# Performance work log

Hardware: AMD Instinct MI355X
Metric: run time of the kernel (lower is better)

## Reference

```python
import jax, jax.numpy as jnp
import numpy as np

B, H, S, D = 4, 16, 2048, 64


def setup_inputs() -> dict:
    key = jax.random.key(0)
    kq, kk, kv = jax.random.split(key, 3)
    q = jax.random.normal(kq, (B, H, S, D), dtype=jnp.float32)
    k = jax.random.normal(kk, (B, H, S, D), dtype=jnp.float32)
    v = jax.random.normal(kv, (B, H, S, D), dtype=jnp.float32)
    # causal mask: 1 = keep, 0 = masked (matches masked_fill(mask == 0, -10000))
    mask = jnp.tril(jnp.ones((S, S), dtype=jnp.int32))[None, None, :, :]
    return {"q": q, "k": k, "v": v, "mask": mask}


def reference(q, k, v, mask):
    head_dim = q.shape[3]
    # [b,h,s,t] attention logits
    attn = jnp.einsum("bhsd,bhtd->bhst", q, k) / jnp.sqrt(jnp.float32(head_dim))
    attn = jnp.where(mask == 0, jnp.float32(-10000.0), attn)
    score = jax.nn.softmax(attn, axis=-1)
    # dropout is identity at inference (eval mode)
    return jnp.einsum("bhst,bhtd->bhsd", score, v)
```

## Files before the change

### kernel.cpp

```cpp
#include <hip/hip_runtime.h>
#include <hip/hip_bf16.h>

typedef __bf16 bf16_t;
typedef bf16_t bf16x8 __attribute__((ext_vector_type(8)));
typedef float  f32x4  __attribute__((ext_vector_type(4)));
typedef float  f32x16 __attribute__((ext_vector_type(16)));
typedef int    i32x4  __attribute__((ext_vector_type(4)));

#define DH 64

__device__ __forceinline__ unsigned pkbf(float a, float b) {
    union { bf16_t h[2]; unsigned u; } z;
    z.h[0] = (bf16_t)a; z.h[1] = (bf16_t)b;
    return z.u;
}

#if defined(__has_builtin)
#  if __has_builtin(__builtin_amdgcn_exp2f)
#    define EXP2F(x) __builtin_amdgcn_exp2f(x)
#  else
#    define EXP2F(x) __expf((x) * 0.69314718056f)
#  endif
#else
#  define EXP2F(x) __expf((x) * 0.69314718056f)
#endif


__global__ __launch_bounds__(256, 2)
void sdpa_fwd(const float* __restrict__ Qg, const float* __restrict__ Kg,
              const float* __restrict__ Vg, float* __restrict__ Og)
{
    __shared__ char lds[2 * 32768];

    const int n  = blockIdx.x;
    const int o  = ((n & 7) << 6) | (n >> 3);
    const int bh = o >> 3;
    const int pr = o & 7;

    const int t   = threadIdx.x;
    const int w   = t >> 6;
    const int l31 = t & 31;
    const int hi  = (t >> 5) & 1;
    const int swk0 = ((l31 ^ (l31 >> 3)) & 7) << 4;
    const int swk1 = (((32 + l31) ^ ((32 + l31) >> 3)) & 7) << 4;

    const size_t hoff = (size_t)bh * 2048 * DH;
    const float* Qh = Qg + hoff;
    const float* Kh = Kg + hoff;
    const float* Vh = Vg + hoff;
    float*       Oh = Og + hoff;

    const int srow = (t >> 3) * 2;
    const int sdc  = t & 7;

    const int p0  = 15 - pr;
    const int nk0 = 2 * p0 + 2;
    const int NS  = 17;

    f32x4 rk[8], rv[8];

    auto keybase = [&](int g) { return ((g < nk0) ? g : g - nk0) * 64; };

    auto loadT = [&](int key0, int half) {
        const float* kp = Kh + (size_t)(key0 + srow) * DH + sdc * 8;
        rk[half*4+0] = *(const f32x4*)kp;        rk[half*4+1] = *(const f32x4*)(kp + 4);
        rk[half*4+2] = *(const f32x4*)(kp + DH); rk[half*4+3] = *(const f32x4*)(kp + DH + 4);
        const float* vp = Vh + (size_t)(key0 + srow) * DH + sdc * 8;
        rv[half*4+0] = *(const f32x4*)vp;        rv[half*4+1] = *(const f32x4*)(vp + 4);
        rv[half*4+2] = *(const f32x4*)(vp + DH); rv[half*4+3] = *(const f32x4*)(vp + DH + 4);
    };
    auto stageT = [&](char* kb_, char* vb_, int half) {
#pragma unroll
        for (int r2 = 0; r2 < 2; ++r2) {
            const int key = srow + r2;
            union { unsigned u[4]; bf16x8 v; } f;
            f.u[0] = pkbf(rk[half*4+r2*2][0],   rk[half*4+r2*2][1]);
            f.u[1] = pkbf(rk[half*4+r2*2][2],   rk[half*4+r2*2][3]);
            f.u[2] = pkbf(rk[half*4+r2*2+1][0], rk[half*4+r2*2+1][1]);
            f.u[3] = pkbf(rk[half*4+r2*2+1][2], rk[half*4+r2*2+1][3]);
            *(bf16x8*)(kb_ + ((key * 128 + sdc * 16) ^ (((key ^ (key >> 3)) & 7) << 4))) = f.v;
        }
#pragma unroll
        for (int jj = 0; jj < 8; ++jj) {
            const int d  = sdc * 8 + jj;
            const float x0 = (jj < 4) ? rv[half*4+0][jj & 3] : rv[half*4+1][jj & 3];
            const float x1 = (jj < 4) ? rv[half*4+2][jj & 3] : rv[half*4+3][jj & 3];
            *(unsigned*)(vb_ + ((d * 128 + srow * 2) ^ (((jj ^ sdc) & 7) << 4)))
                = pkbf(x0, x1);
        }
    };

    const float QSCALE = 0.125f * 1.44269504088896f;

    loadT(keybase(0), 0); loadT(keybase(1), 1);
    stageT(lds, lds + 8192, 0);
    stageT(lds + 16384, lds + 24576, 1);
    loadT(keybase(2), 0); loadT(keybase(3), 1);
    __syncthreads();

    int gt = 0;
    const int stripes[2] = { p0, pr };
    for (int s = 0; s < 2; ++s) {
        const int p    = stripes[s];
        const int h    = 2 * p + 2;
        const int qsb  = p * 128 + w * 32;
        const int qrow = qsb + l31;
        const int ktd  = qsb >> 6;

        bf16x8 qf[4];
#pragma unroll
        for (int sd = 0; sd < 4; ++sd) {
            const float* qp = Qh + (size_t)qrow * DH + sd * 16 + hi * 8;
            f32x4 a = *(const f32x4*)qp;
            f32x4 b = *(const f32x4*)(qp + 4);
            union { unsigned u[4]; bf16x8 v; } f;
            f.u[0] = pkbf(a[0]*QSCALE, a[1]*QSCALE);
            f.u[1] = pkbf(a[2]*QSCALE, a[3]*QSCALE);
            f.u[2] = pkbf(b[0]*QSCALE, b[1]*QSCALE);
            f.u[3] = pkbf(b[2]*QSCALE, b[3]*QSCALE);
            qf[sd] = f.v;
        }

        f32x16 acc0 = {}, acc1 = {};
        float l_run = 0.0f;

        auto doTile = [&](char* kb_, char* vb_, int i) {
            f32x16 tf0 = {}, tf1 = {};
            __builtin_amdgcn_s_setprio(1);
#pragma unroll
            for (int sd = 0; sd < 4; ++sd) {
                const int inner = sd * 32 + hi * 16;
                const bf16x8 k0 = *(const bf16x8*)(kb_ + ((l31 * 128 + inner) ^ swk0));
                const bf16x8 k1 = *(const bf16x8*)(kb_ + (((32 + l31) * 128 + inner) ^ swk1));
                tf0 = __builtin_amdgcn_mfma_f32_32x32x16_bf16(k0, qf[sd], tf0, 0, 0, 0);
                tf1 = __builtin_amdgcn_mfma_f32_32x32x16_bf16(k1, qf[sd], tf1, 0, 0, 0);
            }
            __builtin_amdgcn_s_setprio(0);

            if (i == ktd) {
#pragma unroll
                for (int rr = 0; rr < 16; ++rr) {
                    const int krow = i * 64 + (rr & 3) + 8 * (rr >> 2) + 4 * hi;
                    if (krow > qrow)      tf0[rr] = -20000.0f;
                    if (krow + 32 > qrow) tf1[rr] = -20000.0f;
                }
            }

            float sum = 0.0f;
#pragma unroll
            for (int rr = 0; rr < 16; ++rr) { tf0[rr] = EXP2F(tf0[rr]); sum += tf0[rr]; }
#pragma unroll
            for (int rr = 0; rr < 16; ++rr) { tf1[rr] = EXP2F(tf1[rr]); sum += tf1[rr]; }
            sum += __shfl_xor(sum, 32);
            l_run += sum;

            unsigned P0[2][4], P1[2][4];
#pragma unroll
            for (int rg = 0; rg < 4; ++rg) {
                P0[0][rg] = pkbf(tf0[rg * 4 + 0], tf0[rg * 4 + 1]);
                P1[0][rg] = pkbf(tf0[rg * 4 + 2], tf0[rg * 4 + 3]);
                P0[1][rg] = pkbf(tf1[rg * 4 + 0], tf1[rg * 4 + 1]);
                P1[1][rg] = pkbf(tf1[rg * 4 + 2], tf1[rg * 4 + 3]);
            }

            __builtin_amdgcn_s_setprio(1);
#pragma unroll
            for (int sidx = 0; sidx < 4; ++sidx) {
                const int kb  = sidx >> 1;
                const int rgl = (sidx & 1) * 2, rgh = rgl + 1;
                int w0, w1, w2, w3;
#if defined(__has_builtin) && __has_builtin(__builtin_amdgcn_permlane32_swap)
                auto r0 = __builtin_amdgcn_permlane32_swap((int)P0[kb][rgl], (int)P0[kb][rgh], false, false);
                auto r1 = __builtin_amdgcn_permlane32_swap((int)P1[kb][rgl], (int)P1[kb][rgh], false, false);
                w0 = r0[0]; w2 = r0[1]; w1 = r1[0]; w3 = r1[1];
#else
                const int sa0 = __shfl_xor((int)P0[kb][rgl], 32);
                const int sb0 = __shfl_xor((int)P0[kb][rgh], 32);
                const int sa1 = __shfl_xor((int)P1[kb][rgl], 32);
                const int sb1 = __shfl_xor((int)P1[kb][rgh], 32);
                w0 = hi ? sb0 : (int)P0[kb][rgl];
                w2 = hi ? (int)P0[kb][rgh] : sa0;
                w1 = hi ? sb1 : (int)P1[kb][rgl];
                w3 = hi ? (int)P1[kb][rgh] : sa1;
#endif
                union { i32x4 ii; bf16x8 v; } pz;
                pz.ii = (i32x4){ w0, w1, w2, w3 };

                const int inner = sidx * 32 + hi * 16;
                const int d0 = l31;
                const int d1 = 32 + l31;
                const int sz0 = (((d0 & 7) ^ (d0 >> 3)) & 7) << 4;
                const int sz1 = (((d1 & 7) ^ (d1 >> 3)) & 7) << 4;
                const bf16x8 v0 = *(const bf16x8*)(vb_ + ((d0 * 128 + inner) ^ sz0));
                const bf16x8 v1 = *(const bf16x8*)(vb_ + ((d1 * 128 + inner) ^ sz1));
                acc0 = __builtin_amdgcn_mfma_f32_32x32x16_bf16(v0, pz.v, acc0, 0, 0, 0);
                acc1 = __builtin_amdgcn_mfma_f32_32x32x16_bf16(v1, pz.v, acc1, 0, 0, 0);
            }
            __builtin_amdgcn_s_setprio(0);
        };

        for (int si = 0; si < (h >> 1); ++si, gt += 2) {
            const int gs = gt >> 1;
            char* cb_ = lds + (gs & 1) * 32768;
            char* sb_ = lds + ((gs + 1) & 1) * 32768;

            if (gs + 1 < NS) {
                stageT(sb_, sb_ + 8192, 0);
                stageT(sb_ + 16384, sb_ + 24576, 1);
            }
            if (gs + 2 < NS) {
                loadT(keybase(2 * gs + 4), 0);
                loadT(keybase(2 * gs + 5), 1);
            }

            const int i0 = 2 * si;
            if (i0 <= ktd)     doTile(cb_,          cb_ + 8192,  i0);
            if (i0 + 1 <= ktd) doTile(cb_ + 16384,  cb_ + 24576, i0 + 1);

            __syncthreads();
        }

        const float inv = 1.0f / l_run;
        float* op = Oh + (size_t)qrow * DH;
#pragma unroll
        for (int rq = 0; rq < 4; ++rq) {
            f32x4 o0, o1;
#pragma unroll
            for (int j = 0; j < 4; ++j) {
                o0[j] = acc0[rq * 4 + j] * inv;
                o1[j] = acc1[rq * 4 + j] * inv;
            }
            *(f32x4*)(op + 8 * rq + 4 * hi)      = o0;
            *(f32x4*)(op + 32 + 8 * rq + 4 * hi) = o1;
        }
    }
}

extern "C" void kernel_launch(void* const* d_in, const int* in_sizes, int n_in,
                              void* d_out, int out_size, void* d_ws, size_t ws_size,
                              hipStream_t stream) {
    (void)in_sizes; (void)n_in; (void)d_ws; (void)ws_size; (void)out_size;
    const float* q = (const float*)d_in[0];
    const float* k = (const float*)d_in[1];
    const float* v = (const float*)d_in[2];
    float* out = (float*)d_out;
    hipLaunchKernelGGL(sdpa_fwd, dim3(512), dim3(256), 0, stream, q, k, v, out);
}
```

Before: 70.93 us.

## Process both causal query stripes in one shared K/V pass

Each block previously handled its long and short query stripes one after the other, loading and staging K/V tiles for each stripe separately, which meant 17 staged steps. Now both stripes' Q fragments and accumulators stay live and a single sweep over the K/V tiles feeds both stripes, so the short stripe's tiles are reused from LDS instead of being fetched and converted again. This removes redundant global loads, bf16 conversion and LDS staging. In exchange it doubles the accumulator and Q register footprint, which can cut occupancy or cause spills.

```diff
diff --git a/kernel.cpp b/kernel.cpp
--- a/kernel.cpp
+++ b/kernel.cpp
@@ -53,13 +53,12 @@
     const int srow = (t >> 3) * 2;
     const int sdc  = t & 7;
 
-    const int p0  = 15 - pr;
-    const int nk0 = 2 * p0 + 2;
-    const int NS  = 17;
+    const int pA  = 15 - pr;
+    const int pB  = pr;
+    const int NTt = 2 * pA + 2;
+    const int NS  = NTt >> 1;
 
     f32x4 rk[8], rv[8];
-
-    auto keybase = [&](int g) { return ((g < nk0) ? g : g - nk0) * 64; };
 
     auto loadT = [&](int key0, int half) {
         const float* kp = Kh + (size_t)(key0 + srow) * DH + sdc * 8;
@@ -92,143 +91,163 @@
 
     const float QSCALE = 0.125f * 1.44269504088896f;
 
-    loadT(keybase(0), 0); loadT(keybase(1), 1);
+    const int qsbA = pA * 128 + w * 32, qrowA = qsbA + l31, ktdA = qsbA >> 6;
+    const int qsbB = pB * 128 + w * 32, qrowB = qsbB + l31, ktdB = qsbB >> 6;
+
+    bf16x8 qfA[4], qfB[4];
+#pragma unroll
+    for (int sd = 0; sd < 4; ++sd) {
+        const float* qpA = Qh + (size_t)qrowA * DH + sd * 16 + hi * 8;
+        f32x4 a = *(const f32x4*)qpA;
+        f32x4 b = *(const f32x4*)(qpA + 4);
+        union { unsigned u[4]; bf16x8 v; } f;
+        f.u[0] = pkbf(a[0]*QSCALE, a[1]*QSCALE);
+        f.u[1] = pkbf(a[2]*QSCALE, a[3]*QSCALE);
+        f.u[2] = pkbf(b[0]*QSCALE, b[1]*QSCALE);
+        f.u[3] = pkbf(b[2]*QSCALE, b[3]*QSCALE);
+        qfA[sd] = f.v;
+        const float* qpB = Qh + (size_t)qrowB * DH + sd * 16 + hi * 8;
+        a = *(const f32x4*)qpB;
+        b = *(const f32x4*)(qpB + 4);
+        f.u[0] = pkbf(a[0]*QSCALE, a[1]*QSCALE);
+        f.u[1] = pkbf(a[2]*QSCALE, a[3]*QSCALE);
+        f.u[2] = pkbf(b[0]*QSCALE, b[1]*QSCALE);
+        f.u[3] = pkbf(b[2]*QSCALE, b[3]*QSCALE);
+        qfB[sd] = f.v;
+    }
+
+    f32x16 accA0 = {}, accA1 = {}, accB0 = {}, accB1 = {};
+    float lA = 0.0f, lB = 0.0f;
+
+    auto doTileS = [&](const bf16x8* qf, f32x16& acc0, f32x16& acc1, float& l_run,
+                       int ktd, int qrow, char* kb_, char* vb_, int i) {
+        f32x16 tf0 = {}, tf1 = {};
+        __builtin_amdgcn_s_setprio(1);
+#pragma unroll
+        for (int sd = 0; sd < 4; ++sd) {
+            const int inner = sd * 32 + hi * 16;
+            const bf16x8 k0 = *(const bf16x8*)(kb_ + ((l31 * 128 + inner) ^ swk0));
+            const bf16x8 k1 = *(const bf16x8*)(kb_ + (((32 + l31) * 128 + inner) ^ swk1));
+            tf0 = __builtin_amdgcn_mfma_f32_32x32x16_bf16(k0, qf[sd], tf0, 0, 0, 0);
+            tf1 = __builtin_amdgcn_mfma_f32_32x32x16_bf16(k1, qf[sd], tf1, 0, 0, 0);
+        }
+        __builtin_amdgcn_s_setprio(0);
+
+        if (i == ktd) {
+#pragma unroll
+            for (int rr = 0; rr < 16; ++rr) {
+                const int krow = i * 64 + (rr & 3) + 8 * (rr >> 2) + 4 * hi;
+                if (krow > qrow)      tf0[rr] = -20000.0f;
+                if (krow + 32 > qrow) tf1[rr] = -20000.0f;
+            }
+        }
+
+        float sum = 0.0f;
+#pragma unroll
+        for (int rr = 0; rr < 16; ++rr) { tf0[rr] = EXP2F(tf0[rr]); sum += tf0[rr]; }
+#pragma unroll
+        for (int rr = 0; rr < 16; ++rr) { tf1[rr] = EXP2F(tf1[rr]); sum += tf1[rr]; }
+        sum += __shfl_xor(sum, 32);
+        l_run += sum;
+
+        unsigned P0[2][4], P1[2][4];
+#pragma unroll
+        for (int rg = 0; rg < 4; ++rg) {
+            P0[0][rg] = pkbf(tf0[rg * 4 + 0], tf0[rg * 4 + 1]);
+            P1[0][rg] = pkbf(tf0[rg * 4 + 2], tf0[rg * 4 + 3]);
+            P0[1][rg] = pkbf(tf1[rg * 4 + 0], tf1[rg * 4 + 1]);
+            P1[1][rg] = pkbf(tf1[rg * 4 + 2], tf1[rg * 4 + 3]);
+        }
+
+        __builtin_amdgcn_s_setprio(1);
+#pragma unroll
+        for (int sidx = 0; sidx < 4; ++sidx) {
+            const int kb  = sidx >> 1;
+            const int rgl = (sidx & 1) * 2, rgh = rgl + 1;
+            int w0, w1, w2, w3;
+#if defined(__has_builtin) && __has_builtin(__builtin_amdgcn_permlane32_swap)
+            auto r0 = __builtin_amdgcn_permlane32_swap((int)P0[kb][rgl], (int)P0[kb][rgh], false, false);
+            auto r1 = __builtin_amdgcn_permlane32_swap((int)P1[kb][rgl], (int)P1[kb][rgh], false, false);
+            w0 = r0[0]; w2 = r0[1]; w1 = r1[0]; w3 = r1[1];
+#else
+            const int sa0 = __shfl_xor((int)P0[kb][rgl], 32);
+            const int sb0 = __shfl_xor((int)P0[kb][rgh], 32);
+            const int sa1 = __shfl_xor((int)P1[kb][rgl], 32);
+            const int sb1 = __shfl_xor((int)P1[kb][rgh], 32);
+            w0 = hi ? sb0 : (int)P0[kb][rgl];
+            w2 = hi ? (int)P0[kb][rgh] : sa0;
+            w1 = hi ? sb1 : (int)P1[kb][rgl];
+            w3 = hi ? (int)P1[kb][rgh] : sa1;
+#endif
+            union { i32x4 ii; bf16x8 v; } pz;
+            pz.ii = (i32x4){ w0, w1, w2, w3 };
+
+            const int inner = sidx * 32 + hi * 16;
+            const int d0 = l31;
+            const int d1 = 32 + l31;
+            const int sz0 = (((d0 & 7) ^ (d0 >> 3)) & 7) << 4;
+            const int sz1 = (((d1 & 7) ^ (d1 >> 3)) & 7) << 4;
+            const bf16x8 v0 = *(const bf16x8*)(vb_ + ((d0 * 128 + inner) ^ sz0));
+            const bf16x8 v1 = *(const bf16x8*)(vb_ + ((d1 * 128 + inner) ^ sz1));
+            acc0 = __builtin_amdgcn_mfma_f32_32x32x16_bf16(v0, pz.v, acc0, 0, 0, 0);
+            acc1 = __builtin_amdgcn_mfma_f32_32x32x16_bf16(v1, pz.v, acc1, 0, 0, 0);
+        }
+        __builtin_amdgcn_s_setprio(0);
+    };
+
+    loadT(0, 0);  loadT(64, 1);
     stageT(lds, lds + 8192, 0);
     stageT(lds + 16384, lds + 24576, 1);
-    loadT(keybase(2), 0); loadT(keybase(3), 1);
+    loadT(128, 0); loadT(192, 1);
     __syncthreads();
 
-    int gt = 0;
-    const int stripes[2] = { p0, pr };
-    for (int s = 0; s < 2; ++s) {
-        const int p    = stripes[s];
-        const int h    = 2 * p + 2;
-        const int qsb  = p * 128 + w * 32;
-        const int qrow = qsb + l31;
-        const int ktd  = qsb >> 6;
-
-        bf16x8 qf[4];
-#pragma unroll
-        for (int sd = 0; sd < 4; ++sd) {
-            const float* qp = Qh + (size_t)qrow * DH + sd * 16 + hi * 8;
-            f32x4 a = *(const f32x4*)qp;
-            f32x4 b = *(const f32x4*)(qp + 4);
-            union { unsigned u[4]; bf16x8 v; } f;
-            f.u[0] = pkbf(a[0]*QSCALE, a[1]*QSCALE);
-            f.u[1] = pkbf(a[2]*QSCALE, a[3]*QSCALE);
-            f.u[2] = pkbf(b[0]*QSCALE, b[1]*QSCALE);
-            f.u[3] = pkbf(b[2]*QSCALE, b[3]*QSCALE);
-            qf[sd] = f.v;
-        }
-
-        f32x16 acc0 = {}, acc1 = {};
-        float l_run = 0.0f;
-
-        auto doTile = [&](char* kb_, char* vb_, int i) {
-            f32x16 tf0 = {}, tf1 = {};
-            __builtin_amdgcn_s_setprio(1);
-#pragma unroll
-            for (int sd = 0; sd < 4; ++sd) {
-                const int inner = sd * 32 + hi * 16;
-                const bf16x8 k0 = *(const bf16x8*)(kb_ + ((l31 * 128 + inner) ^ swk0));
-                const bf16x8 k1 = *(const bf16x8*)(kb_ + (((32 + l31) * 128 + inner) ^ swk1));
-                tf0 = __builtin_amdgcn_mfma_f32_32x32x16_bf16(k0, qf[sd], tf0, 0, 0, 0);
-                tf1 = __builtin_amdgcn_mfma_f32_32x32x16_bf16(k1, qf[sd], tf1, 0, 0, 0);
-            }
-            __builtin_amdgcn_s_setprio(0);
-
-            if (i == ktd) {
-#pragma unroll
-                for (int rr = 0; rr < 16; ++rr) {
-                    const int krow = i * 64 + (rr & 3) + 8 * (rr >> 2) + 4 * hi;
-                    if (krow > qrow)      tf0[rr] = -20000.0f;
-                    if (krow + 32 > qrow) tf1[rr] = -20000.0f;
-                }
-            }
-
-            float sum = 0.0f;
-#pragma unroll
-            for (int rr = 0; rr < 16; ++rr) { tf0[rr] = EXP2F(tf0[rr]); sum += tf0[rr]; }
-#pragma unroll
-            for (int rr = 0; rr < 16; ++rr) { tf1[rr] = EXP2F(tf1[rr]); sum += tf1[rr]; }
-            sum += __shfl_xor(sum, 32);
-            l_run += sum;
-
-            unsigned P0[2][4], P1[2][4];
-#pragma unroll
-            for (int rg = 0; rg < 4; ++rg) {
-                P0[0][rg] = pkbf(tf0[rg * 4 + 0], tf0[rg * 4 + 1]);
-                P1[0][rg] = pkbf(tf0[rg * 4 + 2], tf0[rg * 4 + 3]);
-                P0[1][rg] = pkbf(tf1[rg * 4 + 0], tf1[rg * 4 + 1]);
-                P1[1][rg] = pkbf(tf1[rg * 4 + 2], tf1[rg * 4 + 3]);
-            }
-
-            __builtin_amdgcn_s_setprio(1);
-#pragma unroll
-            for (int sidx = 0; sidx < 4; ++sidx) {
-                const int kb  = sidx >> 1;
-                const int rgl = (sidx & 1) * 2, rgh = rgl + 1;
-                int w0, w1, w2, w3;
-#if defined(__has_builtin) && __has_builtin(__builtin_amdgcn_permlane32_swap)
-                auto r0 = __builtin_amdgcn_permlane32_swap((int)P0[kb][rgl], (int)P0[kb][rgh], false, false);
-                auto r1 = __builtin_amdgcn_permlane32_swap((int)P1[kb][rgl], (int)P1[kb][rgh], false, false);
-                w0 = r0[0]; w2 = r0[1]; w1 = r1[0]; w3 = r1[1];
-#else
-                const int sa0 = __shfl_xor((int)P0[kb][rgl], 32);
-                const int sb0 = __shfl_xor((int)P0[kb][rgh], 32);
-                const int sa1 = __shfl_xor((int)P1[kb][rgl], 32);
-                const int sb1 = __shfl_xor((int)P1[kb][rgh], 32);
-                w0 = hi ? sb0 : (int)P0[kb][rgl];
-                w2 = hi ? (int)P0[kb][rgh] : sa0;
-                w1 = hi ? sb1 : (int)P1[kb][rgl];
-                w3 = hi ? (int)P1[kb][rgh] : sa1;
-#endif
-                union { i32x4 ii; bf16x8 v; } pz;
-                pz.ii = (i32x4){ w0, w1, w2, w3 };
-
-                const int inner = sidx * 32 + hi * 16;
-                const int d0 = l31;
-                const int d1 = 32 + l31;
-                const int sz0 = (((d0 & 7) ^ (d0 >> 3)) & 7) << 4;
-                const int sz1 = (((d1 & 7) ^ (d1 >> 3)) & 7) << 4;
-                const bf16x8 v0 = *(const bf16x8*)(vb_ + ((d0 * 128 + inner) ^ sz0));
-                const bf16x8 v1 = *(const bf16x8*)(vb_ + ((d1 * 128 + inner) ^ sz1));
-                acc0 = __builtin_amdgcn_mfma_f32_32x32x16_bf16(v0, pz.v, acc0, 0, 0, 0);
-                acc1 = __builtin_amdgcn_mfma_f32_32x32x16_bf16(v1, pz.v, acc1, 0, 0, 0);
-            }
-            __builtin_amdgcn_s_setprio(0);
-        };
-
-        for (int si = 0; si < (h >> 1); ++si, gt += 2) {
-            const int gs = gt >> 1;
-            char* cb_ = lds + (gs & 1) * 32768;
-            char* sb_ = lds + ((gs + 1) & 1) * 32768;
-
-            if (gs + 1 < NS) {
-                stageT(sb_, sb_ + 8192, 0);
-                stageT(sb_ + 16384, sb_ + 24576, 1);
-            }
-            if (gs + 2 < NS) {
-                loadT(keybase(2 * gs + 4), 0);
-                loadT(keybase(2 * gs + 5), 1);
-            }
-
-            const int i0 = 2 * si;
-            if (i0 <= ktd)     doTile(cb_,          cb_ + 8192,  i0);
-            if (i0 + 1 <= ktd) doTile(cb_ + 16384,  cb_ + 24576, i0 + 1);
-
-            __syncthreads();
-        }
-
-        const float inv = 1.0f / l_run;
-        float* op = Oh + (size_t)qrow * DH;
+    for (int gs = 0; gs < NS; ++gs) {
+        char* cb_ = lds + (gs & 1) * 32768;
+        char* sb_ = lds + ((gs + 1) & 1) * 32768;
+
+        if (gs + 1 < NS) {
+            stageT(sb_, sb_ + 8192, 0);
+            stageT(sb_ + 16384, sb_ + 24576, 1);
+        }
+        if (gs + 2 < NS) {
+            loadT((2 * gs + 4) * 64, 0);
+            loadT((2 * gs + 5) * 64, 1);
+        }
+
+        const int i0 = 2 * gs;
+        if (i0 <= ktdA)     doTileS(qfA, accA0, accA1, lA, ktdA, qrowA, cb_,         cb_ + 8192,  i0);
+        if (i0 <= ktdB)     doTileS(qfB, accB0, accB1, lB, ktdB, qrowB, cb_,         cb_ + 8192,  i0);
+        if (i0 + 1 <= ktdA) doTileS(qfA, accA0, accA1, lA, ktdA, qrowA, cb_ + 16384, cb_ + 24576, i0 + 1);
+        if (i0 + 1 <= ktdB) doTileS(qfB, accB0, accB1, lB, ktdB, qrowB, cb_ + 16384, cb_ + 24576, i0 + 1);
+
+        __syncthreads();
+    }
+
+    {
+        const float inv = 1.0f / lA;
+        float* op = Oh + (size_t)qrowA * DH;
 #pragma unroll
         for (int rq = 0; rq < 4; ++rq) {
             f32x4 o0, o1;
 #pragma unroll
             for (int j = 0; j < 4; ++j) {
-                o0[j] = acc0[rq * 4 + j] * inv;
-                o1[j] = acc1[rq * 4 + j] * inv;
+                o0[j] = accA0[rq * 4 + j] * inv;
+                o1[j] = accA1[rq * 4 + j] * inv;
+            }
+            *(f32x4*)(op + 8 * rq + 4 * hi)      = o0;
+            *(f32x4*)(op + 32 + 8 * rq + 4 * hi) = o1;
+        }
+    }
+    {
+        const float inv = 1.0f / lB;
+        float* op = Oh + (size_t)qrowB * DH;
+#pragma unroll
+        for (int rq = 0; rq < 4; ++rq) {
+            f32x4 o0, o1;
+#pragma unroll
+            for (int j = 0; j < 4; ++j) {
+                o0[j] = accB0[rq * 4 + j] * inv;
+                o1[j] = accB1[rq * 4 + j] * inv;
             }
             *(f32x4*)(op + 8 * rq + 4 * hi)      = o0;
             *(f32x4*)(op + 32 + 8 * rq + 4 * hi) = o1;
```

Measured after the change: 75.19 us. +6.0%, slower.

## Split each tile's keys across warp pairs and merge partial accumulators via LDS

Applied to the files above, without the earlier changes.

Work is repartitioned so each warp handles 64 query rows (two 32-row halves) and one 32-key half of every 64-key tile, instead of 32 query rows over all 64 keys. K fragments are then reused across two query sub-blocks and the causal skip is finer grained, which cuts LDS K reads per warp and evens out load across warps. The cost is extra LDS (about 9 KB), a multi-phase LDS reduction of partial accumulators and row sums with eight extra barriers per stripe, and higher register pressure from four accumulators per warp.

```diff
diff --git a/kernel.cpp b/kernel.cpp
--- a/kernel.cpp
+++ b/kernel.cpp
@@ -30,7 +30,7 @@
 void sdpa_fwd(const float* __restrict__ Qg, const float* __restrict__ Kg,
               const float* __restrict__ Vg, float* __restrict__ Og)
 {
-    __shared__ char lds[2 * 32768];
+    __shared__ char lds[74752];
 
     const int n  = blockIdx.x;
     const int o  = ((n & 7) << 6) | (n >> 3);
@@ -39,10 +39,14 @@
 
     const int t   = threadIdx.x;
     const int w   = t >> 6;
+    const int kh  = w & 1;
+    const int qh  = w >> 1;
+    const int l63 = t & 63;
     const int l31 = t & 31;
     const int hi  = (t >> 5) & 1;
-    const int swk0 = ((l31 ^ (l31 >> 3)) & 7) << 4;
-    const int swk1 = (((32 + l31) ^ ((32 + l31) >> 3)) & 7) << 4;
+
+    const int krow = kh * 32 + l31;
+    const int kswz = ((krow ^ (krow >> 3)) & 7) << 4;
 
     const size_t hoff = (size_t)bh * 2048 * DH;
     const float* Qh = Qg + hoff;
@@ -92,6 +96,10 @@
 
     const float QSCALE = 0.125f * 1.44269504088896f;
 
+    char*  mrgA = lds + 65536;
+    float* mrgL = (float*)(lds + 74240);
+    const int mb = (qh * 64 + l63) * 68;
+
     loadT(keybase(0), 0); loadT(keybase(1), 1);
     stageT(lds, lds + 8192, 0);
     stageT(lds + 16384, lds + 24576, 1);
@@ -101,102 +109,132 @@
     int gt = 0;
     const int stripes[2] = { p0, pr };
     for (int s = 0; s < 2; ++s) {
-        const int p    = stripes[s];
-        const int h    = 2 * p + 2;
-        const int qsb  = p * 128 + w * 32;
-        const int qrow = qsb + l31;
-        const int ktd  = qsb >> 6;
-
-        bf16x8 qf[4];
+        const int p     = stripes[s];
+        const int h     = 2 * p + 2;
+        const int qsb0  = p * 128 + qh * 64;
+        const int qsb1  = qsb0 + 32;
+        const int qrow0 = qsb0 + l31;
+        const int qrow1 = qsb1 + l31;
+
+        bf16x8 qf0[4], qf1[4];
 #pragma unroll
         for (int sd = 0; sd < 4; ++sd) {
-            const float* qp = Qh + (size_t)qrow * DH + sd * 16 + hi * 8;
-            f32x4 a = *(const f32x4*)qp;
-            f32x4 b = *(const f32x4*)(qp + 4);
+            const float* qp0 = Qh + (size_t)qrow0 * DH + sd * 16 + hi * 8;
+            f32x4 a = *(const f32x4*)qp0;
+            f32x4 b = *(const f32x4*)(qp0 + 4);
             union { unsigned u[4]; bf16x8 v; } f;
             f.u[0] = pkbf(a[0]*QSCALE, a[1]*QSCALE);
             f.u[1] = pkbf(a[2]*QSCALE, a[3]*QSCALE);
             f.u[2] = pkbf(b[0]*QSCALE, b[1]*QSCALE);
             f.u[3] = pkbf(b[2]*QSCALE, b[3]*QSCALE);
-            qf[sd] = f.v;
-        }
-
-        f32x16 acc0 = {}, acc1 = {};
-        float l_run = 0.0f;
+            qf0[sd] = f.v;
+            const float* qp1 = Qh + (size_t)qrow1 * DH + sd * 16 + hi * 8;
+            a = *(const f32x4*)qp1;
+            b = *(const f32x4*)(qp1 + 4);
+            f.u[0] = pkbf(a[0]*QSCALE, a[1]*QSCALE);
+            f.u[1] = pkbf(a[2]*QSCALE, a[3]*QSCALE);
+            f.u[2] = pkbf(b[0]*QSCALE, b[1]*QSCALE);
+            f.u[3] = pkbf(b[2]*QSCALE, b[3]*QSCALE);
+            qf1[sd] = f.v;
+        }
+
+        f32x16 a00 = {}, a01 = {};
+        f32x16 a10 = {}, a11 = {};
+        float l0 = 0.0f, l1 = 0.0f;
 
         auto doTile = [&](char* kb_, char* vb_, int i) {
-            f32x16 tf0 = {}, tf1 = {};
-            __builtin_amdgcn_s_setprio(1);
-#pragma unroll
-            for (int sd = 0; sd < 4; ++sd) {
-                const int inner = sd * 32 + hi * 16;
-                const bf16x8 k0 = *(const bf16x8*)(kb_ + ((l31 * 128 + inner) ^ swk0));
-                const bf16x8 k1 = *(const bf16x8*)(kb_ + (((32 + l31) * 128 + inner) ^ swk1));
-                tf0 = __builtin_amdgcn_mfma_f32_32x32x16_bf16(k0, qf[sd], tf0, 0, 0, 0);
-                tf1 = __builtin_amdgcn_mfma_f32_32x32x16_bf16(k1, qf[sd], tf1, 0, 0, 0);
-            }
-            __builtin_amdgcn_s_setprio(0);
-
-            if (i == ktd) {
-#pragma unroll
-                for (int rr = 0; rr < 16; ++rr) {
-                    const int krow = i * 64 + (rr & 3) + 8 * (rr >> 2) + 4 * hi;
-                    if (krow > qrow)      tf0[rr] = -20000.0f;
-                    if (krow + 32 > qrow) tf1[rr] = -20000.0f;
-                }
-            }
-
-            float sum = 0.0f;
-#pragma unroll
-            for (int rr = 0; rr < 16; ++rr) { tf0[rr] = EXP2F(tf0[rr]); sum += tf0[rr]; }
-#pragma unroll
-            for (int rr = 0; rr < 16; ++rr) { tf1[rr] = EXP2F(tf1[rr]); sum += tf1[rr]; }
-            sum += __shfl_xor(sum, 32);
-            l_run += sum;
-
-            unsigned P0[2][4], P1[2][4];
-#pragma unroll
-            for (int rg = 0; rg < 4; ++rg) {
-                P0[0][rg] = pkbf(tf0[rg * 4 + 0], tf0[rg * 4 + 1]);
-                P1[0][rg] = pkbf(tf0[rg * 4 + 2], tf0[rg * 4 + 3]);
-                P0[1][rg] = pkbf(tf1[rg * 4 + 0], tf1[rg * 4 + 1]);
-                P1[1][rg] = pkbf(tf1[rg * 4 + 2], tf1[rg * 4 + 3]);
-            }
-
-            __builtin_amdgcn_s_setprio(1);
-#pragma unroll
-            for (int sidx = 0; sidx < 4; ++sidx) {
-                const int kb  = sidx >> 1;
-                const int rgl = (sidx & 1) * 2, rgh = rgl + 1;
-                int w0, w1, w2, w3;
-#if defined(__has_builtin) && __has_builtin(__builtin_amdgcn_permlane32_swap)
-                auto r0 = __builtin_amdgcn_permlane32_swap((int)P0[kb][rgl], (int)P0[kb][rgh], false, false);
-                auto r1 = __builtin_amdgcn_permlane32_swap((int)P1[kb][rgl], (int)P1[kb][rgh], false, false);
-                w0 = r0[0]; w2 = r0[1]; w1 = r1[0]; w3 = r1[1];
-#else
-                const int sa0 = __shfl_xor((int)P0[kb][rgl], 32);
-                const int sb0 = __shfl_xor((int)P0[kb][rgh], 32);
-                const int sa1 = __shfl_xor((int)P1[kb][rgl], 32);
-                const int sb1 = __shfl_xor((int)P1[kb][rgh], 32);
-                w0 = hi ? sb0 : (int)P0[kb][rgl];
-                w2 = hi ? (int)P0[kb][rgh] : sa0;
-                w1 = hi ? sb1 : (int)P1[kb][rgl];
-                w3 = hi ? (int)P1[kb][rgh] : sa1;
-#endif
-                union { i32x4 ii; bf16x8 v; } pz;
-                pz.ii = (i32x4){ w0, w1, w2, w3 };
-
-                const int inner = sidx * 32 + hi * 16;
-                const int d0 = l31;
-                const int d1 = 32 + l31;
+            const int kb0 = i * 64 + kh * 32;
+            if (kb0 > qsb1 + 31) return;
+            const bool b0 = (kb0 <= qsb0 + 31);
+
+            bf16x8 kf[4];
+#pragma unroll
+            for (int sd = 0; sd < 4; ++sd)
+                kf[sd] = *(const bf16x8*)(kb_ + ((krow * 128 + sd * 32 + hi * 16) ^ kswz));
+            bf16x8 vf00, vf01, vf10, vf11;
+            {
+                const int d0 = l31, d1 = 32 + l31;
                 const int sz0 = (((d0 & 7) ^ (d0 >> 3)) & 7) << 4;
                 const int sz1 = (((d1 & 7) ^ (d1 >> 3)) & 7) << 4;
-                const bf16x8 v0 = *(const bf16x8*)(vb_ + ((d0 * 128 + inner) ^ sz0));
-                const bf16x8 v1 = *(const bf16x8*)(vb_ + ((d1 * 128 + inner) ^ sz1));
-                acc0 = __builtin_amdgcn_mfma_f32_32x32x16_bf16(v0, pz.v, acc0, 0, 0, 0);
-                acc1 = __builtin_amdgcn_mfma_f32_32x32x16_bf16(v1, pz.v, acc1, 0, 0, 0);
-            }
+                const int base = kh * 64 + hi * 16;
+                vf00 = *(const bf16x8*)(vb_ + ((d0 * 128 + base) ^ sz0));
+                vf01 = *(const bf16x8*)(vb_ + ((d0 * 128 + base + 32) ^ sz0));
+                vf10 = *(const bf16x8*)(vb_ + ((d1 * 128 + base) ^ sz1));
+                vf11 = *(const bf16x8*)(vb_ + ((d1 * 128 + base + 32) ^ sz1));
+            }
+
+            auto finish = [&](f32x16& tf, float& lr, f32x16& A0, f32x16& A1) {
+                float sum = 0.0f;
+#pragma unroll
+                for (int rr = 0; rr < 16; ++rr) { tf[rr] = EXP2F(tf[rr]); sum += tf[rr]; }
+                sum += __shfl_xor(sum, 32);
+                lr += sum;
+                unsigned P0[4], P1[4];
+#pragma unroll
+                for (int rg = 0; rg < 4; ++rg) {
+                    P0[rg] = pkbf(tf[rg * 4 + 0], tf[rg * 4 + 1]);
+                    P1[rg] = pkbf(tf[rg * 4 + 2], tf[rg * 4 + 3]);
+                }
+                __builtin_amdgcn_s_setprio(1);
+#pragma unroll
+                for (int sc = 0; sc < 2; ++sc) {
+                    const int rgl = sc * 2, rgh = rgl + 1;
+                    int w0, w1, w2, w3;
+#if defined(__has_builtin) && __has_builtin(__builtin_amdgcn_permlane32_swap)
+                    auto r0 = __builtin_amdgcn_permlane32_swap((int)P0[rgl], (int)P0[rgh], false, false);
+                    auto r1 = __builtin_amdgcn_permlane32_swap((int)P1[rgl], (int)P1[rgh], false, false);
+                    w0 = r0[0]; w2 = r0[1]; w1 = r1[0]; w3 = r1[1];
+#else
+                    const int sa0 = __shfl_xor((int)P0[rgl], 32);
+                    const int sb0 = __shfl_xor((int)P0[rgh], 32);
+                    const int sa1 = __shfl_xor((int)P1[rgl], 32);
+                    const int sb1 = __shfl_xor((int)P1[rgh], 32);
+                    w0 = hi ? sb0 : (int)P0[rgl];
+                    w2 = hi ? (int)P0[rgh] : sa0;
+                    w1 = hi ? sb1 : (int)P1[rgl];
+                    w3 = hi ? (int)P1[rgh] : sa1;
+#endif
+                    union { i32x4 ii; bf16x8 v; } pz;
+                    pz.ii = (i32x4){ w0, w1, w2, w3 };
+                    const bf16x8 v0 = sc ? vf01 : vf00;
+                    const bf16x8 v1 = sc ? vf11 : vf10;
+                    A0 = __builtin_amdgcn_mfma_f32_32x32x16_bf16(v0, pz.v, A0, 0, 0, 0);
+                    A1 = __builtin_amdgcn_mfma_f32_32x32x16_bf16(v1, pz.v, A1, 0, 0, 0);
+                }
+                __builtin_amdgcn_s_setprio(0);
+            };
+
+            f32x16 tf1 = {};
+            __builtin_amdgcn_s_setprio(1);
+#pragma unroll
+            for (int sd = 0; sd < 4; ++sd)
+                tf1 = __builtin_amdgcn_mfma_f32_32x32x16_bf16(kf[sd], qf1[sd], tf1, 0, 0, 0);
             __builtin_amdgcn_s_setprio(0);
+            if (kb0 + 31 > qsb1) {
+#pragma unroll
+                for (int rr = 0; rr < 16; ++rr) {
+                    const int kr = kb0 + (rr & 3) + 8 * (rr >> 2) + 4 * hi;
+                    if (kr > qrow1) tf1[rr] = -20000.0f;
+                }
+            }
+            finish(tf1, l1, a10, a11);
+
+            if (b0) {
+                f32x16 tf0 = {};
+                __builtin_amdgcn_s_setprio(1);
+#pragma unroll
+                for (int sd = 0; sd < 4; ++sd)
+                    tf0 = __builtin_amdgcn_mfma_f32_32x32x16_bf16(kf[sd], qf0[sd], tf0, 0, 0, 0);
+                __builtin_amdgcn_s_setprio(0);
+                if (kb0 + 31 > qsb0) {
+#pragma unroll
+                    for (int rr = 0; rr < 16; ++rr) {
+                        const int kr = kb0 + (rr & 3) + 8 * (rr >> 2) + 4 * hi;
+                        if (kr > qrow0) tf0[rr] = -20000.0f;
+                    }
+                }
+                finish(tf0, l0, a00, a01);
+            }
         };
 
         for (int si = 0; si < (h >> 1); ++si, gt += 2) {
@@ -214,25 +252,71 @@
             }
 
             const int i0 = 2 * si;
-            if (i0 <= ktd)     doTile(cb_,          cb_ + 8192,  i0);
-            if (i0 + 1 <= ktd) doTile(cb_ + 16384,  cb_ + 24576, i0 + 1);
+            doTile(cb_,         cb_ + 8192,  i0);
+            doTile(cb_ + 16384, cb_ + 24576, i0 + 1);
 
             __syncthreads();
         }
 
-        const float inv = 1.0f / l_run;
-        float* op = Oh + (size_t)qrow * DH;
-#pragma unroll
-        for (int rq = 0; rq < 4; ++rq) {
-            f32x4 o0, o1;
+        auto mput = [&](const f32x16& A) {
 #pragma unroll
             for (int j = 0; j < 4; ++j) {
-                o0[j] = acc0[rq * 4 + j] * inv;
-                o1[j] = acc1[rq * 4 + j] * inv;
-            }
-            *(f32x4*)(op + 8 * rq + 4 * hi)      = o0;
-            *(f32x4*)(op + 32 + 8 * rq + 4 * hi) = o1;
-        }
+                f32x4 c = { A[j*4+0], A[j*4+1], A[j*4+2], A[j*4+3] };
+                *(f32x4*)(mrgA + mb + j * 16) = c;
+            }
+        };
+        auto mget = [&](f32x16& A) {
+#pragma unroll
+            for (int j = 0; j < 4; ++j) {
+                const f32x4 c = *(const f32x4*)(mrgA + mb + j * 16);
+#pragma unroll
+                for (int r2 = 0; r2 < 4; ++r2) A[j*4+r2] += c[r2];
+            }
+        };
+        if (kh) { mput(a00); mrgL[qh * 64 + l63] = l0; }
+        __syncthreads();
+        if (!kh) { mget(a00); l0 += mrgL[qh * 64 + l63]; }
+        __syncthreads();
+        if (kh) mput(a01);
+        __syncthreads();
+        if (!kh) mget(a01);
+        __syncthreads();
+        if (kh) { mput(a10); mrgL[qh * 64 + l63] = l1; }
+        __syncthreads();
+        if (!kh) { mget(a10); l1 += mrgL[qh * 64 + l63]; }
+        __syncthreads();
+        if (kh) mput(a11);
+        __syncthreads();
+        if (!kh) {
+            mget(a11);
+            const float i0v = 1.0f / l0;
+            float* op0 = Oh + (size_t)qrow0 * DH;
+#pragma unroll
+            for (int rq = 0; rq < 4; ++rq) {
+                f32x4 o0, o1;
+#pragma unroll
+                for (int j = 0; j < 4; ++j) {
+                    o0[j] = a00[rq * 4 + j] * i0v;
+                    o1[j] = a01[rq * 4 + j] * i0v;
+                }
+                *(f32x4*)(op0 + 8 * rq + 4 * hi)      = o0;
+                *(f32x4*)(op0 + 32 + 8 * rq + 4 * hi) = o1;
+            }
+            const float i1v = 1.0f / l1;
+            float* op1 = Oh + (size_t)qrow1 * DH;
+#pragma unroll
+            for (int rq = 0; rq < 4; ++rq) {
+                f32x4 o0, o1;
+#pragma unroll
+                for (int j = 0; j < 4; ++j) {
+                    o0[j] = a10[rq * 4 + j] * i1v;
+                    o1[j] = a11[rq * 4 + j] * i1v;
+                }
+                *(f32x4*)(op1 + 8 * rq + 4 * hi)      = o0;
+                *(f32x4*)(op1 + 32 + 8 * rq + 4 * hi) = o1;
+            }
+        }
+        __syncthreads();
     }
 }
 
```

New measurement: 82.75 us. +16.7%, slower.
